# Optimization experiments

Hardware: AMD Instinct MI355X
Metric: run time of the kernel (lower is better)

Reference implementation:

```python
import jax, jax.numpy as jnp
import numpy as np

NUM_BUCKETS = 320
MAX_DISTANCE = 800


def _layer_norm(x, w, b, eps=1e-5):
    x32 = x.astype(jnp.float32)
    mu = x32.mean(-1, keepdims=True)
    var = x32.var(-1, keepdims=True)
    return ((x32 - mu) / jnp.sqrt(var + eps) * w + b).astype(x.dtype)


def _rel_pos_bucket(rel):
    half = NUM_BUCKETS // 2            # 160
    st = half // 2                     # 80 (small threshold)
    sign = (rel >= 0).astype(jnp.int32)
    ab = jnp.abs(rel)
    is_small = ab < st
    log_ratio = jnp.log(jnp.clip(ab.astype(jnp.float32), 1.0) / st) / np.float32(np.log(MAX_DISTANCE / st))
    log_pos = st + (log_ratio * (half - st)).astype(jnp.int32)  # trunc toward zero like .long()
    log_pos = jnp.minimum(log_pos, half - 1)
    bucket = jnp.where(is_small, ab, log_pos) + sign * half
    return jnp.clip(bucket, 0, NUM_BUCKETS - 1)


def setup_inputs() -> dict:
    key = jax.random.key(0)
    B, T, C, H, FF = 2, 2048, 768, 12, 3072
    D = C // H
    ks = jax.random.split(key, 16)
    s = 0.02
    return {
        "x": jax.random.normal(ks[0], (B, T, C), jnp.float32),
        "ln1_w": jnp.ones((C,), jnp.float32),
        "ln1_b": jnp.zeros((C,), jnp.float32),
        "wq": jax.random.normal(ks[1], (C, C), jnp.float32) * s,
        "bq": jnp.zeros((C,), jnp.float32),
        "wk": jax.random.normal(ks[2], (C, C), jnp.float32) * s,
        "bk": jnp.zeros((C,), jnp.float32),
        "wv": jax.random.normal(ks[3], (C, C), jnp.float32) * s,
        "bv": jnp.zeros((C,), jnp.float32),
        "wo": jax.random.normal(ks[4], (C, C), jnp.float32) * s,
        "bo": jnp.zeros((C,), jnp.float32),
        "ln2_w": jnp.ones((C,), jnp.float32),
        "ln2_b": jnp.zeros((C,), jnp.float32),
        "w1": jax.random.normal(ks[5], (FF, C), jnp.float32) * s,
        "b1": jnp.zeros((FF,), jnp.float32),
        "w2": jax.random.normal(ks[6], (C, FF), jnp.float32) * s,
        "b2": jnp.zeros((C,), jnp.float32),
        "rel_embed": jax.random.normal(ks[7], (NUM_BUCKETS, H), jnp.float32),
        "gate_ur_w": jax.random.normal(ks[8], (H, D), jnp.float32) * 0.01,
        "gate_i_w": jax.random.normal(ks[9], (H, D), jnp.float32) * 0.01,
        "rel_scale": jnp.ones((H,), jnp.float32),
    }


def reference(x, ln1_w, ln1_b, wq, bq, wk, bk, wv, bv, wo, bo,
              ln2_w, ln2_b, w1, b1, w2, b2, rel_embed, gate_ur_w, gate_i_w, rel_scale):
    B, T, C = x.shape
    H = rel_embed.shape[1]
    D = C // H

    residual = x
    h = _layer_norm(x, ln1_w, ln1_b)
    q = (h @ wq.T + bq).reshape(B, T, H, D).transpose(0, 2, 1, 3)  # [B,H,T,D]
    k = (h @ wk.T + bk).reshape(B, T, H, D).transpose(0, 2, 1, 3)
    v = (h @ wv.T + bv).reshape(B, T, H, D).transpose(0, 2, 1, 3)

    attn = jnp.einsum('bhqd,bhkd->bhqk', q, k) * (D ** -0.5)

    # gated relative position bias
    pos = jnp.arange(T)
    rel = pos[None, :] - pos[:, None]                 # [T,T]
    buckets = _rel_pos_bucket(rel)                    # [T,T]
    pe = rel_embed[buckets]                           # [T,T,H]
    pe = jnp.transpose(pe, (2, 0, 1))[None]           # [1,H,T,T]
    g_in = q.mean(axis=2).transpose(0, 2, 1).mean(axis=-1)   # [B,D]
    gate_r = jax.nn.sigmoid(g_in @ gate_ur_w.T)       # [B,H]
    gate_u = jax.nn.sigmoid(g_in @ gate_i_w.T)        # [B,H]
    gate = 1.0 + (gate_u * rel_scale[None, :] * gate_r)[:, :, None, None]
    bias = pe * gate                                  # [B,H,T,T]

    attn = jax.nn.softmax(attn + bias, axis=-1)
    out = jnp.einsum('bhqk,bhkd->bhqd', attn, v).transpose(0, 2, 1, 3).reshape(B, T, C)
    x = residual + out @ wo.T + bo

    residual = x
    h = _layer_norm(x, ln2_w, ln2_b)
    h = jax.nn.gelu(h @ w1.T + b1, approximate=False) @ w2.T + b2
    return residual + h
```

## Files before the change

kernel.cpp:

```cpp
#include <hip/hip_runtime.h>
#include <hip/hip_bf16.h>


#define Tn 2048
#define Cn 768
#define Hn 12
#define Dn 64
#define FFn 3072
#define Mn 4096
#define QKVS 2304
#define LQK 1536

typedef __attribute__((ext_vector_type(8))) short bfrag;
typedef __attribute__((ext_vector_type(8))) unsigned short us8;
typedef __attribute__((ext_vector_type(4))) float f32x4;

#define GLDS(gptr, lptr) __builtin_amdgcn_global_load_lds( \
    (const __attribute__((address_space(1))) void*)(gptr), \
    (__attribute__((address_space(3))) void*)(lptr), 16, 0, 0)

#define SBAR()   __builtin_amdgcn_s_barrier()
#define WAITVM4() asm volatile("s_waitcnt vmcnt(4)" ::: "memory")
#define WAITVM0() asm volatile("s_waitcnt vmcnt(0)" ::: "memory")
#define WAITLG0() asm volatile("s_waitcnt lgkmcnt(0)" ::: "memory")

#define QSCALE 0.18033688f
#define INVQS  5.5451774445f

__device__ __forceinline__ unsigned short f2bu(float f){
  __hip_bfloat16 h = __float2bfloat16(f);
  return *(unsigned short*)&h;
}
__device__ __forceinline__ float bu2f(unsigned short u){
  union { unsigned int i; float f; } v; v.i = ((unsigned int)u) << 16; return v.f;
}
__device__ __forceinline__ us8 pack8(float4 a, float4 b){
  us8 c;
  c[0]=f2bu(a.x); c[1]=f2bu(a.y); c[2]=f2bu(a.z); c[3]=f2bu(a.w);
  c[4]=f2bu(b.x); c[5]=f2bu(b.y); c[6]=f2bu(b.z); c[7]=f2bu(b.w);
  return c;
}
__device__ __forceinline__ float fexp2(float x){ return __builtin_amdgcn_exp2f(x); }

__device__ __forceinline__ float block_reduce_sum(float v, float* sred){
  #pragma unroll
  for (int off = 32; off > 0; off >>= 1) v += __shfl_down(v, off, 64);
  __syncthreads();
  if ((threadIdx.x & 63) == 0) sred[threadIdx.x >> 6] = v;
  __syncthreads();
  return sred[0] + sred[1] + sred[2] + sred[3];
}

__global__ __launch_bounds__(256) void cast_all_kernel(
    const float* __restrict__ wq, const float* __restrict__ wk,
    const float* __restrict__ wv, const float* __restrict__ wo,
    const float* __restrict__ w1, const float* __restrict__ w2,
    const float* __restrict__ bq, const float* __restrict__ bk,
    const float* __restrict__ bv, const float* __restrict__ rel_embed,
    unsigned short* __restrict__ Wqkv, unsigned short* __restrict__ Wob,
    unsigned short* __restrict__ W1b, unsigned short* __restrict__ W2b,
    float* __restrict__ bias_rel, float* __restrict__ bqkv)
{
  const int blk = blockIdx.x;
  if (blk >= 3472){
    const int i = (blk - 3472) * 256 + threadIdx.x;
    bqkv[i] = (i < Cn) ? bq[i] : (i < 2 * Cn) ? bk[i - Cn] : bv[i - 2 * Cn];
    return;
  }
  if (blk >= 3456){
    const int idx = (blk - 3456) * 256 + threadIdx.x;
    if (idx >= 4095) return;
    const int rel = idx - 2047;
    const int ab = rel < 0 ? -rel : rel;
    int bucket;
    if (ab < 80){
      bucket = ab;
    } else {
      const float lr = logf((float)ab * (1.0f / 80.0f)) * (1.0f / 2.3025851f);
      int lp = 80 + (int)(lr * 80.0f);
      bucket = lp < 159 ? lp : 159;
    }
    if (rel >= 0) bucket += 160;
    #pragma unroll
    for (int h = 0; h < Hn; h++)
      bias_rel[h * 4095 + idx] = rel_embed[bucket * Hn + h] * 1.44269504089f;
    return;
  }
  const float* src; unsigned short* dst; int i;
  if (blk < 288)      { src = wq; dst = Wqkv;               i = blk * 256 + threadIdx.x; }
  else if (blk < 576) { src = wk; dst = Wqkv + Cn * Cn;     i = (blk - 288) * 256 + threadIdx.x; }
  else if (blk < 864) { src = wv; dst = Wqkv + 2 * Cn * Cn; i = (blk - 576) * 256 + threadIdx.x; }
  else if (blk < 1152){ src = wo; dst = Wob;                i = (blk - 864) * 256 + threadIdx.x; }
  else if (blk < 2304){ src = w1; dst = W1b;                i = (blk - 1152) * 256 + threadIdx.x; }
  else                { src = w2; dst = W2b;                i = (blk - 2304) * 256 + threadIdx.x; }
  const float4 a = ((const float4*)src)[i * 2];
  const float4 b = ((const float4*)src)[i * 2 + 1];
  *(us8*)&dst[i * 8] = pack8(a, b);
}

__global__ __launch_bounds__(256) void ln_kernel(const float* __restrict__ xin,
    const float* __restrict__ w, const float* __restrict__ bsh,
    unsigned short* __restrict__ out)
{
  __shared__ float xs[Cn];
  __shared__ float sred[4];
  const size_t base = (size_t)blockIdx.x * Cn;
  float s = 0.f;
  for (int c = threadIdx.x; c < Cn; c += 256){
    float v = xin[base + c];
    xs[c] = v; s += v;
  }
  const float mean = block_reduce_sum(s, sred) * (1.f / Cn);
  float s2 = 0.f;
  for (int c = threadIdx.x; c < Cn; c += 256){
    float d = xs[c] - mean; s2 += d * d;
  }
  const float var = block_reduce_sum(s2, sred) * (1.f / Cn);
  const float rstd = rsqrtf(var + 1e-5f);
  for (int c = threadIdx.x; c < Cn; c += 256)
    out[base + c] = f2bu((xs[c] - mean) * rstd * w[c] + bsh[c]);
}

template<int EPI, bool TRANSV>
__global__ __launch_bounds__(256) void gemm_mfma_kernel(
    const unsigned short* __restrict__ A, const unsigned short* __restrict__ Bw,
    const float* __restrict__ bias, unsigned short* __restrict__ vt,
    void* __restrict__ Cout, int M, int N, int K, int ldo)
{
  __shared__ __align__(16) unsigned short As[2][128 * 32];
  __shared__ __align__(16) unsigned short Bs[2][128 * 32];
  const int tid = threadIdx.x;
  const int lane = tid & 63, w = tid >> 6;
  const int nl = lane & 15, quad = lane >> 4;
  const int wm = w >> 1, wn = w & 1;
  const int id = blockIdx.x;
  const int bm = ((id & 7) * 4 + ((id >> 3) & 3)) * 128;
  const int bn = (id >> 5) * 128;
  const int l4 = lane >> 2;
  const int lk = (((lane & 3) ^ ((lane >> 3) & 3)) * 8);
  const int qsw = (quad ^ ((nl >> 1) & 3)) * 8;

  f32x4 acc[4][4];
  #pragma unroll
  for (int i = 0; i < 4; i++)
    #pragma unroll
    for (int j = 0; j < 4; j++) acc[i][j] = (f32x4){0.f, 0.f, 0.f, 0.f};

  const int c0 = w, c1 = w + 4;
  const unsigned short* A0 = A + (size_t)(bm + c0 * 16 + l4) * K + lk;
  const unsigned short* A1 = A + (size_t)(bm + c1 * 16 + l4) * K + lk;
  const unsigned short* B0 = Bw + (size_t)(bn + c0 * 16 + l4) * K + lk;
  const unsigned short* B1 = Bw + (size_t)(bn + c1 * 16 + l4) * K + lk;

  GLDS(A0, &As[0][c0 * 512]); GLDS(A1, &As[0][c1 * 512]);
  GLDS(B0, &Bs[0][c0 * 512]); GLDS(B1, &Bs[0][c1 * 512]);

  const int NIT = K >> 5;
  for (int t = 0; t < NIT; t++){
    const int cur = t & 1;
    SBAR();
    if (t + 1 < NIT){
      const int k0 = (t + 1) << 5;
      GLDS(A0 + k0, &As[cur ^ 1][c0 * 512]);
      GLDS(A1 + k0, &As[cur ^ 1][c1 * 512]);
      GLDS(B0 + k0, &Bs[cur ^ 1][c0 * 512]);
      GLDS(B1 + k0, &Bs[cur ^ 1][c1 * 512]);
      WAITVM4();
    } else {
      WAITVM0();
    }
    SBAR();
    bfrag Af[4], Bf[4];
    #pragma unroll
    for (int mt = 0; mt < 4; mt++)
      Af[mt] = *(const bfrag*)&As[cur][(wm * 64 + mt * 16 + nl) * 32 + qsw];
    #pragma unroll
    for (int nt = 0; nt < 4; nt++)
      Bf[nt] = *(const bfrag*)&Bs[cur][(wn * 64 + nt * 16 + nl) * 32 + qsw];
    #pragma unroll
    for (int mt = 0; mt < 4; mt++)
      #pragma unroll
      for (int nt = 0; nt < 4; nt++)
        acc[mt][nt] = __builtin_amdgcn_mfma_f32_16x16x32_bf16(Af[mt], Bf[nt], acc[mt][nt], 0, 0, 0);
  }

  if (TRANSV && bn >= 1536){
    #pragma unroll
    for (int nt = 0; nt < 4; nt++){
      const int col = bn + wn * 64 + nt * 16 + nl;
      const float bv_ = bias[col];
      const int vcol = col - 1536;
      #pragma unroll
      for (int mt = 0; mt < 4; mt++){
        const int row0 = bm + wm * 64 + mt * 16 + quad * 4;
        unsigned short pk[4];
        #pragma unroll
        for (int r = 0; r < 4; r++) pk[r] = f2bu(acc[mt][nt][r] + bv_);
        *(uint2*)&vt[(size_t)vcol * Mn + row0] = *(uint2*)pk;
      }
    }
    return;
  }
  #pragma unroll
  for (int nt = 0; nt < 4; nt++){
    const int col = bn + wn * 64 + nt * 16 + nl;
    const float bv_ = bias[col];
    const float sc = (EPI == 1 && col < Cn) ? QSCALE : 1.0f;
    #pragma unroll
    for (int mt = 0; mt < 4; mt++){
      const int row0 = bm + wm * 64 + mt * 16 + quad * 4;
      #pragma unroll
      for (int r = 0; r < 4; r++){
        const size_t idx = (size_t)(row0 + r) * ldo + col;
        const float v = acc[mt][nt][r] + bv_;
        if (EPI == 2){
          ((unsigned short*)Cout)[idx] = f2bu(0.5f * v * (1.f + erff(v * 0.70710678118f)));
        } else {
          ((unsigned short*)Cout)[idx] = f2bu(v * sc);
        }
      }
    }
  }
}

__global__ __launch_bounds__(256) void gemm_t64_kernel(
    const unsigned short* __restrict__ A, const unsigned short* __restrict__ Bw,
    const float* __restrict__ bias, const float* __restrict__ res,
    float* __restrict__ Cout, int M, int N, int K)
{
  __shared__ __align__(16) unsigned short As[2][2 * 64 * 32];
  __shared__ __align__(16) unsigned short Bs[2][2 * 64 * 32];
  const int tid = threadIdx.x;
  const int lane = tid & 63, w = tid >> 6;
  const int nl = lane & 15, quad = lane >> 4;
  const int id = blockIdx.x;
  const int bm = ((id & 7) * 8 + ((id >> 3) & 7)) * 64;
  const int bn = (id >> 6) * 64;
  const int l2 = lane >> 2;
  const int l3 = (((lane & 3) ^ ((lane >> 3) & 3)) * 8);
  const int qsw = (quad ^ ((nl >> 1) & 3)) * 8;

  f32x4 acc[4];
  #pragma unroll
  for (int j = 0; j < 4; j++) acc[j] = (f32x4){0.f, 0.f, 0.f, 0.f};

  const unsigned short* A0 = A + (size_t)(bm + w * 16 + l2) * K + l3;
  const unsigned short* B0 = Bw + (size_t)(bn + w * 16 + l2) * K + l3;

  GLDS(A0,      &As[0][w * 512]);
  GLDS(A0 + 32, &As[0][2048 + w * 512]);
  GLDS(B0,      &Bs[0][w * 512]);
  GLDS(B0 + 32, &Bs[0][2048 + w * 512]);

  const int NIT = K >> 6;
  for (int t = 0; t < NIT; t++){
    const int cur = t & 1;
    SBAR();
    if (t + 1 < NIT){
      const int k0 = (t + 1) << 6;
      GLDS(A0 + k0,      &As[cur ^ 1][w * 512]);
      GLDS(A0 + k0 + 32, &As[cur ^ 1][2048 + w * 512]);
      GLDS(B0 + k0,      &Bs[cur ^ 1][w * 512]);
      GLDS(B0 + k0 + 32, &Bs[cur ^ 1][2048 + w * 512]);
      WAITVM4();
    } else {
      WAITVM0();
    }
    SBAR();
    const bfrag Af0 = *(const bfrag*)&As[cur][(w * 16 + nl) * 32 + qsw];
    const bfrag Af1 = *(const bfrag*)&As[cur][2048 + (w * 16 + nl) * 32 + qsw];
    bfrag Bf0[4], Bf1[4];
    #pragma unroll
    for (int nt = 0; nt < 4; nt++){
      Bf0[nt] = *(const bfrag*)&Bs[cur][(nt * 16 + nl) * 32 + qsw];
      Bf1[nt] = *(const bfrag*)&Bs[cur][2048 + (nt * 16 + nl) * 32 + qsw];
    }
    #pragma unroll
    for (int nt = 0; nt < 4; nt++){
      acc[nt] = __builtin_amdgcn_mfma_f32_16x16x32_bf16(Af0, Bf0[nt], acc[nt], 0, 0, 0);
      acc[nt] = __builtin_amdgcn_mfma_f32_16x16x32_bf16(Af1, Bf1[nt], acc[nt], 0, 0, 0);
    }
  }

  const int row0 = bm + w * 16 + quad * 4;
  #pragma unroll
  for (int nt = 0; nt < 4; nt++){
    const int col = bn + nt * 16 + nl;
    const float bv_ = bias[col];
    #pragma unroll
    for (int r = 0; r < 4; r++){
      const size_t idx = (size_t)(row0 + r) * N + col;
      Cout[idx] = acc[nt][r] + bv_ + res[idx];
    }
  }
}

__global__ __launch_bounds__(256) void qmean_part_kernel(
    const unsigned short* __restrict__ QKVqk, float* __restrict__ qpart)
{
  __shared__ float ps[Cn];
  const int b = blockIdx.y, t0 = blockIdx.x * 128;
  const int tid = threadIdx.x;
  float a0 = 0.f, a1 = 0.f, a2 = 0.f;
  for (int r = 0; r < 128; r++){
    const size_t base = (size_t)(b * Tn + t0 + r) * LQK;
    a0 += bu2f(QKVqk[base + tid]);
    a1 += bu2f(QKVqk[base + tid + 256]);
    a2 += bu2f(QKVqk[base + tid + 512]);
  }
  ps[tid] = a0; ps[tid + 256] = a1; ps[tid + 512] = a2;
  __syncthreads();
  if (tid < Dn){
    float s = 0.f;
    #pragma unroll
    for (int hh = 0; hh < Hn; hh++) s += ps[hh * Dn + tid];
    qpart[(b * 16 + blockIdx.x) * Dn + tid] = s;
  }
}

__global__ __launch_bounds__(64) void gate_kernel(const float* __restrict__ qpart,
    const float* __restrict__ gur, const float* __restrict__ gi,
    const float* __restrict__ rsc, float* __restrict__ gate)
{
  const int b = blockIdx.x / Hn, h = blockIdx.x % Hn;
  const int d = threadIdx.x;
  float s = 0.f;
  #pragma unroll
  for (int blk = 0; blk < 16; blk++) s += qpart[(b * 16 + blk) * Dn + d];
  const float g = s * (1.f / (Hn * Tn)) * INVQS;
  float vr = g * gur[h * Dn + d];
  float vu = g * gi[h * Dn + d];
  #pragma unroll
  for (int off = 32; off > 0; off >>= 1){
    vr += __shfl_down(vr, off, 64);
    vu += __shfl_down(vu, off, 64);
  }
  if (d == 0){
    const float gr = 1.f / (1.f + __expf(-vr));
    const float gu = 1.f / (1.f + __expf(-vu));
    gate[blockIdx.x] = 1.f + gu * rsc[h] * gr;
  }
}

__global__ __launch_bounds__(256) void attn_mfma_kernel(
    const unsigned short* __restrict__ QKVqk, const unsigned short* __restrict__ VT,
    const float* __restrict__ bias_rel, const float* __restrict__ gate,
    unsigned short* __restrict__ O)
{
  __shared__ __align__(16) char smem[52224];
  unsigned short* Qs = (unsigned short*)smem;
  float* bias_blk    = (float*)smem;
  unsigned short* KsP = (unsigned short*)(smem + 9216);
  unsigned short* VtP = (unsigned short*)(smem + 25600);
  unsigned short* Ptq = (unsigned short*)(smem + 41984);
  float* lsh         = (float*)(smem + 51200);

  const int qbase = blockIdx.x * 64;
  const int h = blockIdx.y, b = blockIdx.z;
  const int tid = threadIdx.x;
  const float g = gate[b * Hn + h];
  const float* brow = bias_rel + h * 4095 + 1984 - qbase;
  const unsigned short* Q = QKVqk;
  const unsigned short* K = QKVqk + Cn;

  const int lane = tid & 63, w = tid >> 6;
  const int nl = lane & 15, quad = lane >> 4;
  const int l2 = lane >> 2;
  const int l3 = (((lane & 3) ^ ((lane >> 3) & 3)) * 8);
  const int qsw = (quad ^ ((nl >> 1) & 3)) * 8;

  const unsigned short* kg0 = K + (size_t)(b * Tn + w * 16 + l2) * LQK + h * Dn + l3;
  const unsigned short* vg0 = VT + (size_t)(h * Dn + w * 16 + l2) * Mn + (size_t)b * Tn + l3;

  GLDS(kg0,      KsP + w * 512);
  GLDS(kg0 + 32, KsP + 2048 + w * 512);
  GLDS(vg0,      VtP + w * 512);
  GLDS(vg0 + 32, VtP + 2048 + w * 512);

  {
    const int row = tid >> 2, cg = (tid & 3) * 16;
    const us8* qp = (const us8*)(Q + (size_t)(b * Tn + qbase + row) * LQK + h * Dn + cg);
    *(us8*)&Qs[row * 72 + cg]     = qp[0];
    *(us8*)&Qs[row * 72 + cg + 8] = qp[1];
  }
  __syncthreads();

  bfrag Qb[4][2];
  #pragma unroll
  for (int mt = 0; mt < 4; mt++){
    Qb[mt][0] = *(const bfrag*)&Qs[(mt * 16 + nl) * 72 + quad * 8];
    Qb[mt][1] = *(const bfrag*)&Qs[(mt * 16 + nl) * 72 + 32 + quad * 8];
  }
  __syncthreads();
  for (int j = tid; j < 2111; j += 256) bias_blk[j] = brow[j] * g;
  WAITLG0();

  const int wq = w & 1, wd = w >> 1;
  f32x4 Oa[2][2];
  #pragma unroll
  for (int a = 0; a < 2; a++)
    #pragma unroll
    for (int d0 = 0; d0 < 2; d0++) Oa[a][d0] = (f32x4){0.f, 0.f, 0.f, 0.f};
  float l_part[4] = {0.f, 0.f, 0.f, 0.f};

  for (int kt = 0; kt < 32; kt++){
    const int kbase = kt * 64;
    const int cur = (kt & 1) * 4096;
    const int nxt = 4096 - cur;
    SBAR();
    if (kt < 31){
      const unsigned short* kg = kg0 + (size_t)(kbase + 64) * LQK;
      const unsigned short* vg = vg0 + kbase + 64;
      GLDS(kg,      KsP + nxt + w * 512);
      GLDS(kg + 32, KsP + nxt + 2048 + w * 512);
      GLDS(vg,      VtP + nxt + w * 512);
      GLDS(vg + 32, VtP + nxt + 2048 + w * 512);
      WAITVM4();
    } else {
      WAITVM0();
    }

    const bfrag Ka0 = *(const bfrag*)&KsP[cur + (w * 16 + nl) * 32 + qsw];
    const bfrag Ka1 = *(const bfrag*)&KsP[cur + 2048 + (w * 16 + nl) * 32 + qsw];
    const int bofs = kbase + w * 16 + quad * 4 + 63 - nl;
    #pragma unroll
    for (int mt = 0; mt < 4; mt++){
      const float* bp = &bias_blk[bofs - mt * 16];
      f32x4 z = (f32x4){bp[0], bp[1], bp[2], bp[3]};
      z = __builtin_amdgcn_mfma_f32_16x16x32_bf16(Ka0, Qb[mt][0], z, 0, 0, 0);
      z = __builtin_amdgcn_mfma_f32_16x16x32_bf16(Ka1, Qb[mt][1], z, 0, 0, 0);
      const float p0 = fexp2(z[0]), p1 = fexp2(z[1]);
      const float p2 = fexp2(z[2]), p3 = fexp2(z[3]);
      l_part[mt] += (p0 + p1) + (p2 + p3);
      uint2 pk2;
      asm("v_cvt_pk_bf16_f32 %0, %1, %2" : "=v"(pk2.x) : "v"(p0), "v"(p1));
      asm("v_cvt_pk_bf16_f32 %0, %1, %2" : "=v"(pk2.y) : "v"(p2), "v"(p3));
      *(uint2*)&Ptq[(mt * 16 + nl) * 72 + w * 16 + quad * 4] = pk2;
    }
    WAITLG0();
    SBAR();

    bfrag Vf[2][2], Pf[2][2];
    #pragma unroll
    for (int d0 = 0; d0 < 2; d0++){
      const int dt = wd * 2 + d0;
      Vf[d0][0] = *(const bfrag*)&VtP[cur + (dt * 16 + nl) * 32 + qsw];
      Vf[d0][1] = *(const bfrag*)&VtP[cur + 2048 + (dt * 16 + nl) * 32 + qsw];
    }
    #pragma unroll
    for (int a = 0; a < 2; a++){
      const int qt = wq * 2 + a;
      Pf[a][0] = *(const bfrag*)&Ptq[(qt * 16 + nl) * 72 + quad * 8];
      Pf[a][1] = *(const bfrag*)&Ptq[(qt * 16 + nl) * 72 + 32 + quad * 8];
    }
    #pragma unroll
    for (int a = 0; a < 2; a++)
      #pragma unroll
      for (int d0 = 0; d0 < 2; d0++){
        Oa[a][d0] = __builtin_amdgcn_mfma_f32_16x16x32_bf16(Vf[d0][0], Pf[a][0], Oa[a][d0], 0, 0, 0);
        Oa[a][d0] = __builtin_amdgcn_mfma_f32_16x16x32_bf16(Vf[d0][1], Pf[a][1], Oa[a][d0], 0, 0, 0);
      }
  }

  #pragma unroll
  for (int mt = 0; mt < 4; mt++){
    float l = l_part[mt];
    l += __shfl_xor(l, 16, 64);
    l += __shfl_xor(l, 32, 64);
    if (quad == 0) lsh[w * 64 + mt * 16 + nl] = l;
  }
  __syncthreads();
  #pragma unroll
  for (int a = 0; a < 2; a++){
    const int q = (wq * 2 + a) * 16 + nl;
    const float linv = 1.f / (lsh[q] + lsh[64 + q] + lsh[128 + q] + lsh[192 + q]);
    unsigned short* orow = O + (size_t)(b * Tn + qbase + q) * Cn + h * Dn;
    #pragma unroll
    for (int d0 = 0; d0 < 2; d0++){
      unsigned short pk[4];
      #pragma unroll
      for (int r = 0; r < 4; r++) pk[r] = f2bu(Oa[a][d0][r] * linv);
      *(uint2*)&orow[(wd * 2 + d0) * 16 + quad * 4] = *(uint2*)pk;
    }
  }
}

extern "C" void kernel_launch(void* const* d_in, const int* in_sizes, int n_in,
                              void* d_out, int out_size, void* d_ws, size_t ws_size,
                              hipStream_t stream)
{
  const float* x     = (const float*)d_in[0];
  const float* ln1_w = (const float*)d_in[1];
  const float* ln1_b = (const float*)d_in[2];
  const float* wq    = (const float*)d_in[3];
  const float* bq    = (const float*)d_in[4];
  const float* wk    = (const float*)d_in[5];
  const float* bk    = (const float*)d_in[6];
  const float* wv    = (const float*)d_in[7];
  const float* bv    = (const float*)d_in[8];
  const float* wo    = (const float*)d_in[9];
  const float* bo    = (const float*)d_in[10];
  const float* ln2_w = (const float*)d_in[11];
  const float* ln2_b = (const float*)d_in[12];
  const float* w1    = (const float*)d_in[13];
  const float* b1    = (const float*)d_in[14];
  const float* w2    = (const float*)d_in[15];
  const float* b2    = (const float*)d_in[16];
  const float* rel_embed = (const float*)d_in[17];
  const float* gur   = (const float*)d_in[18];
  const float* gi    = (const float*)d_in[19];
  const float* rsc   = (const float*)d_in[20];

  char* ws = (char*)d_ws;
  unsigned short* QKVqk = (unsigned short*)(ws);
  unsigned short* VT    = (unsigned short*)(ws + 12582912);
  unsigned short* Ob    = (unsigned short*)(ws + 18874368);
  float*          X2    = (float*)(ws + 25165824);
  unsigned short* Hb    = (unsigned short*)(ws + 37748736);
  unsigned short* Wqkv  = (unsigned short*)(ws + 44040192);
  unsigned short* Wob   = (unsigned short*)(ws + 47579136);
  unsigned short* W1b   = (unsigned short*)(ws + 48758784);
  unsigned short* W2b   = (unsigned short*)(ws + 53477376);
  float*          bqkv  = (float*)(ws + 58195968);
  float*          bias_rel = (float*)(ws + 58205184);
  float*          qpart = (float*)(ws + 58401744);
  float*          gate  = (float*)(ws + 58409936);
  unsigned short* Fb    = (unsigned short*)(ws);

  cast_all_kernel<<<3481, 256, 0, stream>>>(wq, wk, wv, wo, w1, w2, bq, bk, bv,
                                            rel_embed, Wqkv, Wob, W1b, W2b,
                                            bias_rel, bqkv);
  ln_kernel<<<Mn, 256, 0, stream>>>(x, ln1_w, ln1_b, Hb);
  gemm_mfma_kernel<1, true><<<(QKVS / 128) * (Mn / 128), 256, 0, stream>>>(
      Hb, Wqkv, bqkv, VT, QKVqk, Mn, QKVS, Cn, LQK);
  qmean_part_kernel<<<dim3(16, 2), 256, 0, stream>>>(QKVqk, qpart);
  gate_kernel<<<2 * Hn, 64, 0, stream>>>(qpart, gur, gi, rsc, gate);
  attn_mfma_kernel<<<dim3(Tn / 64, Hn, 2), 256, 0, stream>>>(QKVqk, VT, bias_rel, gate, Ob);
  gemm_t64_kernel<<<(Cn / 64) * (Mn / 64), 256, 0, stream>>>(
      Ob, Wob, bo, x, X2, Mn, Cn, Cn);
  ln_kernel<<<Mn, 256, 0, stream>>>(X2, ln2_w, ln2_b, Hb);
  gemm_mfma_kernel<2, false><<<(FFn / 128) * (Mn / 128), 256, 0, stream>>>(
      Hb, W1b, b1, nullptr, Fb, Mn, FFn, Cn, FFn);
  gemm_t64_kernel<<<(Cn / 64) * (Mn / 64), 256, 0, stream>>>(
      Fb, W2b, b2, X2, (float*)d_out, Mn, Cn, FFn);
}
```

Measured before the change: 322.4 us.

## Software-pipeline attention PV step with double-buffered P and register-direct V loads

The attention kernel stops staging V^T in LDS and loads each wave's V fragments straight from global memory into registers, one iteration ahead. The P tile is double-buffered in LDS so the PV MFMAs for the previous key tile run at the start of the next iteration. This removes the mid-iteration barrier and overlaps PV with QK/exp work, with s_setprio raising MFMA priority. In exchange it uses more registers, makes uncoalesced global V reads per wave, and needs a drain step after the loop.

Result: no change. 325.7 us (+1.0%).

```diff
diff --git a/kernel.cpp b/kernel.cpp
--- a/kernel.cpp
+++ b/kernel.cpp
@@ -20,8 +20,7 @@
     (__attribute__((address_space(3))) void*)(lptr), 16, 0, 0)
 
 #define SBAR()   __builtin_amdgcn_s_barrier()
-#define WAITVM4() asm volatile("s_waitcnt vmcnt(4)" ::: "memory")
-#define WAITVM0() asm volatile("s_waitcnt vmcnt(0)" ::: "memory")
+#define WAITVM(N) asm volatile("s_waitcnt vmcnt(" #N ")" ::: "memory")
 #define WAITLG0() asm volatile("s_waitcnt lgkmcnt(0)" ::: "memory")
 
 #define QSCALE 0.18033688f
@@ -165,9 +164,9 @@
       GLDS(A1 + k0, &As[cur ^ 1][c1 * 512]);
       GLDS(B0 + k0, &Bs[cur ^ 1][c0 * 512]);
       GLDS(B1 + k0, &Bs[cur ^ 1][c1 * 512]);
-      WAITVM4();
+      WAITVM(4);
     } else {
-      WAITVM0();
+      WAITVM(0);
     }
     SBAR();
     bfrag Af[4], Bf[4];
@@ -262,9 +261,9 @@
       GLDS(A0 + k0 + 32, &As[cur ^ 1][2048 + w * 512]);
       GLDS(B0 + k0,      &Bs[cur ^ 1][w * 512]);
       GLDS(B0 + k0 + 32, &Bs[cur ^ 1][2048 + w * 512]);
-      WAITVM4();
+      WAITVM(4);
     } else {
-      WAITVM0();
+      WAITVM(0);
     }
     SBAR();
     const bfrag Af0 = *(const bfrag*)&As[cur][(w * 16 + nl) * 32 + qsw];
@@ -347,13 +346,12 @@
     const float* __restrict__ bias_rel, const float* __restrict__ gate,
     unsigned short* __restrict__ O)
 {
-  __shared__ __align__(16) char smem[52224];
+  __shared__ __align__(16) char smem[45056];
   unsigned short* Qs = (unsigned short*)smem;
   float* bias_blk    = (float*)smem;
   unsigned short* KsP = (unsigned short*)(smem + 9216);
-  unsigned short* VtP = (unsigned short*)(smem + 25600);
-  unsigned short* Ptq = (unsigned short*)(smem + 41984);
-  float* lsh         = (float*)(smem + 51200);
+  unsigned short* Ptq = (unsigned short*)(smem + 25600);
+  float* lsh         = (float*)(smem + 44032);
 
   const int qbase = blockIdx.x * 64;
   const int h = blockIdx.y, b = blockIdx.z;
@@ -370,12 +368,12 @@
   const int qsw = (quad ^ ((nl >> 1) & 3)) * 8;
 
   const unsigned short* kg0 = K + (size_t)(b * Tn + w * 16 + l2) * LQK + h * Dn + l3;
-  const unsigned short* vg0 = VT + (size_t)(h * Dn + w * 16 + l2) * Mn + (size_t)b * Tn + l3;
+  const int wq = w & 1, wd = w >> 1;
+  const unsigned short* vrow0 = VT + (size_t)(h * Dn + wd * 32 + nl) * Mn
+                                   + (size_t)b * Tn + quad * 8;
 
   GLDS(kg0,      KsP + w * 512);
   GLDS(kg0 + 32, KsP + 2048 + w * 512);
-  GLDS(vg0,      VtP + w * 512);
-  GLDS(vg0 + 32, VtP + 2048 + w * 512);
 
   {
     const int row = tid >> 2, cg = (tid & 3) * 16;
@@ -395,34 +393,58 @@
   for (int j = tid; j < 2111; j += 256) bias_blk[j] = brow[j] * g;
   WAITLG0();
 
-  const int wq = w & 1, wd = w >> 1;
   f32x4 Oa[2][2];
   #pragma unroll
   for (int a = 0; a < 2; a++)
     #pragma unroll
     for (int d0 = 0; d0 < 2; d0++) Oa[a][d0] = (f32x4){0.f, 0.f, 0.f, 0.f};
   float l_part[4] = {0.f, 0.f, 0.f, 0.f};
+  bfrag Vc[2][2];
 
   for (int kt = 0; kt < 32; kt++){
     const int kbase = kt * 64;
-    const int cur = (kt & 1) * 4096;
-    const int nxt = 4096 - cur;
+    const int curK = (kt & 1) * 4096;
+    const int curP = (kt & 1) * 4608;
+    const int prvP = 4608 - curP;
     SBAR();
+
+    bfrag Vn[2][2];
+    Vn[0][0] = *(const bfrag*)(vrow0 + kbase);
+    Vn[0][1] = *(const bfrag*)(vrow0 + kbase + 32);
+    Vn[1][0] = *(const bfrag*)(vrow0 + (size_t)16 * Mn + kbase);
+    Vn[1][1] = *(const bfrag*)(vrow0 + (size_t)16 * Mn + kbase + 32);
     if (kt < 31){
       const unsigned short* kg = kg0 + (size_t)(kbase + 64) * LQK;
-      const unsigned short* vg = vg0 + kbase + 64;
-      GLDS(kg,      KsP + nxt + w * 512);
-      GLDS(kg + 32, KsP + nxt + 2048 + w * 512);
-      GLDS(vg,      VtP + nxt + w * 512);
-      GLDS(vg + 32, VtP + nxt + 2048 + w * 512);
-      WAITVM4();
+      GLDS(kg,      KsP + (4096 - curK) + w * 512);
+      GLDS(kg + 32, KsP + (4096 - curK) + 2048 + w * 512);
+      WAITVM(6);
     } else {
-      WAITVM0();
-    }
-
-    const bfrag Ka0 = *(const bfrag*)&KsP[cur + (w * 16 + nl) * 32 + qsw];
-    const bfrag Ka1 = *(const bfrag*)&KsP[cur + 2048 + (w * 16 + nl) * 32 + qsw];
+      WAITVM(4);
+    }
+
+    if (kt > 0){
+      bfrag Pf[2][2];
+      #pragma unroll
+      for (int a = 0; a < 2; a++){
+        const int qt = wq * 2 + a;
+        Pf[a][0] = *(const bfrag*)&Ptq[prvP + (qt * 16 + nl) * 72 + quad * 8];
+        Pf[a][1] = *(const bfrag*)&Ptq[prvP + (qt * 16 + nl) * 72 + 32 + quad * 8];
+      }
+      __builtin_amdgcn_s_setprio(1);
+      #pragma unroll
+      for (int a = 0; a < 2; a++)
+        #pragma unroll
+        for (int d0 = 0; d0 < 2; d0++){
+          Oa[a][d0] = __builtin_amdgcn_mfma_f32_16x16x32_bf16(Vc[d0][0], Pf[a][0], Oa[a][d0], 0, 0, 0);
+          Oa[a][d0] = __builtin_amdgcn_mfma_f32_16x16x32_bf16(Vc[d0][1], Pf[a][1], Oa[a][d0], 0, 0, 0);
+        }
+      __builtin_amdgcn_s_setprio(0);
+    }
+
+    const bfrag Ka0 = *(const bfrag*)&KsP[curK + (w * 16 + nl) * 32 + qsw];
+    const bfrag Ka1 = *(const bfrag*)&KsP[curK + 2048 + (w * 16 + nl) * 32 + qsw];
     const int bofs = kbase + w * 16 + quad * 4 + 63 - nl;
+    __builtin_amdgcn_s_setprio(1);
     #pragma unroll
     for (int mt = 0; mt < 4; mt++){
       const float* bp = &bias_blk[bofs - mt * 16];
@@ -435,31 +457,35 @@
       uint2 pk2;
       asm("v_cvt_pk_bf16_f32 %0, %1, %2" : "=v"(pk2.x) : "v"(p0), "v"(p1));
       asm("v_cvt_pk_bf16_f32 %0, %1, %2" : "=v"(pk2.y) : "v"(p2), "v"(p3));
-      *(uint2*)&Ptq[(mt * 16 + nl) * 72 + w * 16 + quad * 4] = pk2;
-    }
+      *(uint2*)&Ptq[curP + (mt * 16 + nl) * 72 + w * 16 + quad * 4] = pk2;
+    }
+    __builtin_amdgcn_s_setprio(0);
     WAITLG0();
-    SBAR();
-
-    bfrag Vf[2][2], Pf[2][2];
-    #pragma unroll
-    for (int d0 = 0; d0 < 2; d0++){
-      const int dt = wd * 2 + d0;
-      Vf[d0][0] = *(const bfrag*)&VtP[cur + (dt * 16 + nl) * 32 + qsw];
-      Vf[d0][1] = *(const bfrag*)&VtP[cur + 2048 + (dt * 16 + nl) * 32 + qsw];
-    }
+
+    Vc[0][0] = Vn[0][0]; Vc[0][1] = Vn[0][1];
+    Vc[1][0] = Vn[1][0]; Vc[1][1] = Vn[1][1];
+  }
+
+  SBAR();
+  WAITVM(0);
+  {
+    const int prvP = 4608;
+    bfrag Pf[2][2];
     #pragma unroll
     for (int a = 0; a < 2; a++){
       const int qt = wq * 2 + a;
-      Pf[a][0] = *(const bfrag*)&Ptq[(qt * 16 + nl) * 72 + quad * 8];
-      Pf[a][1] = *(const bfrag*)&Ptq[(qt * 16 + nl) * 72 + 32 + quad * 8];
-    }
+      Pf[a][0] = *(const bfrag*)&Ptq[prvP + (qt * 16 + nl) * 72 + quad * 8];
+      Pf[a][1] = *(const bfrag*)&Ptq[prvP + (qt * 16 + nl) * 72 + 32 + quad * 8];
+    }
+    __builtin_amdgcn_s_setprio(1);
     #pragma unroll
     for (int a = 0; a < 2; a++)
       #pragma unroll
       for (int d0 = 0; d0 < 2; d0++){
-        Oa[a][d0] = __builtin_amdgcn_mfma_f32_16x16x32_bf16(Vf[d0][0], Pf[a][0], Oa[a][d0], 0, 0, 0);
-        Oa[a][d0] = __builtin_amdgcn_mfma_f32_16x16x32_bf16(Vf[d0][1], Pf[a][1], Oa[a][d0], 0, 0, 0);
+        Oa[a][d0] = __builtin_amdgcn_mfma_f32_16x16x32_bf16(Vc[d0][0], Pf[a][0], Oa[a][d0], 0, 0, 0);
+        Oa[a][d0] = __builtin_amdgcn_mfma_f32_16x16x32_bf16(Vc[d0][1], Pf[a][1], Oa[a][d0], 0, 0, 0);
       }
+    __builtin_amdgcn_s_setprio(0);
   }
 
   #pragma unroll
```
